# Kernel tuning notes

Hardware: AMD Instinct MI355X
Metric: run time of the kernel (lower is better)

Reference implementation:

```python
import jax, jax.numpy as jnp
import numpy as np

N_HEAD = 16
ROPE_BASE = 10000.0


def _rope_tables(T, head_dim, dtype=jnp.float32):
    inv_freq = 1.0 / (ROPE_BASE ** (jnp.arange(0, head_dim, 2, dtype=jnp.float32) / head_dim))
    t = jnp.arange(T, dtype=jnp.float32)
    freqs = t[:, None] * inv_freq[None, :]          # [T, D/2]
    emb = jnp.concatenate([freqs, freqs], axis=-1)  # [T, D]
    return jnp.cos(emb).astype(dtype), jnp.sin(emb).astype(dtype)


def _rotate_half(x):
    d = x.shape[-1] // 2
    return jnp.concatenate([-x[..., d:], x[..., :d]], axis=-1)


def setup_inputs() -> dict:
    key = jax.random.key(0)
    ks = jax.random.split(key, 5)
    B, T, C = 2, 2048, 2048
    s = 1.0 / np.sqrt(C)
    return {
        "x": jax.random.normal(ks[0], (B, T, C), dtype=jnp.float32),
        "wq": jax.random.normal(ks[1], (C, C), dtype=jnp.float32) * s,
        "wk": jax.random.normal(ks[2], (C, C), dtype=jnp.float32) * s,
        "wv": jax.random.normal(ks[3], (C, C), dtype=jnp.float32) * s,
        "wo": jax.random.normal(ks[4], (C, C), dtype=jnp.float32) * s,
    }


def reference(x, wq, wk, wv, wo):
    B, T, C = x.shape
    H = N_HEAD
    D = C // H

    def heads(y):  # [B,T,C] -> [B,H,T,D]
        return y.reshape(B, T, H, D).transpose(0, 2, 1, 3)

    q = heads(x @ wq)
    k = heads(x @ wk)
    v = heads(x @ wv)

    cos, sin = _rope_tables(T, D, x.dtype)          # [T, D]
    cos = cos[None, None, :, :]
    sin = sin[None, None, :, :]
    q = q * cos + _rotate_half(q) * sin
    k = k * cos + _rotate_half(k) * sin

    scale = 1.0 / np.sqrt(D)
    scores = jnp.einsum('bhqd,bhkd->bhqk', q, k) * scale   # [B,H,T,T]
    causal = jnp.tril(jnp.ones((T, T), dtype=bool))
    scores = jnp.where(causal[None, None, :, :], scores, jnp.finfo(scores.dtype).min)
    attn = jax.nn.softmax(scores, axis=-1)
    y = jnp.einsum('bhqk,bhkd->bhqd', attn, v)             # [B,H,T,D]
    y = y.transpose(0, 2, 1, 3).reshape(B, T, C)
    return y @ wo
```

## Files before the change

kernel.cpp:

```cpp
#include <hip/hip_runtime.h>
#include <hip/hip_bf16.h>
#include <math.h>


#define TT 2048
#define CCn 2048
#define HH 16
#define DD 128
#define MMr 4096
#define NQKV 6144

typedef __attribute__((ext_vector_type(8))) short s16x8;
typedef __attribute__((ext_vector_type(4))) short s16x4;
typedef __attribute__((ext_vector_type(4))) float f32x4;

__device__ __forceinline__ short bf16_of(float f) {
  unsigned u = __float_as_uint(f);
  unsigned r = u + 0x7fffu + ((u >> 16) & 1u);
  return (short)(r >> 16);
}
__device__ __forceinline__ float f_of_bf16(short s) {
  return __uint_as_float(((unsigned)(unsigned short)s) << 16);
}
__device__ __forceinline__ float ex2(float x) { return exp2f(x); }

__device__ __forceinline__ void lds_load16(const void* g, void* l) {
  __builtin_amdgcn_global_load_lds((__attribute__((address_space(1))) void*)g,
                                   (__attribute__((address_space(3))) void*)l,
                                   16, 0, 0);
}

__global__ __launch_bounds__(256) void k_tables(float* __restrict__ cosT,
                                                float* __restrict__ sinT) {
  int idx = blockIdx.x * 256 + threadIdx.x;
  int t = idx >> 6, i = idx & 63;
  float inv = powf(10000.0f, -(float)i * (1.0f / 64.0f));
  float f = (float)t * inv;
  cosT[idx] = cosf(f);
  sinT[idx] = sinf(f);
}

__global__ __launch_bounds__(256) void k_cast_x(const float* __restrict__ x,
                                                short* __restrict__ xb) {
  int i = blockIdx.x * 256 + threadIdx.x;
  f32x4 v = ((const f32x4*)x)[i];
  s16x4 o;
#pragma unroll
  for (int j = 0; j < 4; ++j) o[j] = bf16_of(v[j]);
  ((s16x4*)xb)[i] = o;
}

__global__ __launch_bounds__(256) void k_wtrans4(const float* __restrict__ w0,
                                                 const float* __restrict__ w1,
                                                 const float* __restrict__ w2,
                                                 const float* __restrict__ w3,
                                                 short* __restrict__ wqkvT,
                                                 short* __restrict__ woT) {
  __shared__ float tile[32][33];
  int z = blockIdx.z;
  const float* w = (z == 0) ? w0 : (z == 1) ? w1 : (z == 2) ? w2 : w3;
  short* wt = (z == 3) ? woT : wqkvT + (size_t)z * 2048 * 2048;
  int n0 = blockIdx.x * 32, k0 = blockIdx.y * 32;
  int tx = threadIdx.x & 31, ty = threadIdx.x >> 5;
#pragma unroll
  for (int j = 0; j < 4; ++j) {
    int k = ty * 4 + j;
    tile[k][tx] = w[(size_t)(k0 + k) * CCn + n0 + tx];
  }
  __syncthreads();
#pragma unroll
  for (int j = 0; j < 4; ++j) {
    int n = ty * 4 + j;
    wt[(size_t)(n0 + n) * CCn + k0 + tx] = bf16_of(tile[tx][n]);
  }
}

__global__ __launch_bounds__(256) void k_vtrans(const short* __restrict__ src,
                                                short* __restrict__ dst) {
  __shared__ short tile[32][33];
  int bh = blockIdx.y, b = bh >> 4, h = bh & 15;
  int dt = blockIdx.x & 3, tt = blockIdx.x >> 2;
  int tx = threadIdx.x & 31, ty = threadIdx.x >> 5;
  const short* sp = src + ((size_t)(b * TT + tt * 32)) * NQKV + 4096 + h * DD + dt * 32;
#pragma unroll
  for (int j = 0; j < 4; ++j) {
    int tr = ty * 4 + j;
    tile[tr][tx] = sp[(size_t)tr * NQKV + tx];
  }
  __syncthreads();
  short* dp = dst + ((size_t)(bh * DD + dt * 32)) * TT + tt * 32;
#pragma unroll
  for (int j = 0; j < 4; ++j) {
    int dr = ty * 4 + j;
    dp[(size_t)dr * TT + tx] = tile[tx][dr];
  }
}

__global__ __launch_bounds__(256) void k_rope2(const short* __restrict__ qkv,
                                               const float* __restrict__ cosT,
                                               const float* __restrict__ sinT,
                                               short* __restrict__ Qb,
                                               short* __restrict__ Kb, float kmul) {
  int which = blockIdx.y;
  int coff = which << 11;
  short* dstb = which ? Kb : Qb;
  float mul = which ? kmul : 1.0f;
  int idx = blockIdx.x * 256 + threadIdx.x;
  int i4 = (idx & 15) * 4;
  int h = (idx >> 4) & 15;
  int t = (idx >> 8) & 2047;
  int b = idx >> 19;
  const short* row = qkv + ((size_t)(b * TT + t)) * NQKV + coff + h * DD;
  s16x4 v0 = *(const s16x4*)(row + i4);
  s16x4 v1 = *(const s16x4*)(row + i4 + 64);
  f32x4 c4 = *(const f32x4*)(cosT + t * 64 + i4);
  f32x4 s4 = *(const f32x4*)(sinT + t * 64 + i4);
  s16x4 o0, o1;
#pragma unroll
  for (int j = 0; j < 4; ++j) {
    float a = f_of_bf16(v0[j]), bb = f_of_bf16(v1[j]);
    o0[j] = bf16_of((a * c4[j] - bb * s4[j]) * mul);
    o1[j] = bf16_of((bb * c4[j] + a * s4[j]) * mul);
  }
  short* orow = dstb + ((size_t)((b * HH + h) * TT + t)) * DD;
  *(s16x4*)(orow + i4) = o0;
  *(s16x4*)(orow + i4 + 64) = o1;
}

template <int WNF, bool BF16OUT>
__global__ __launch_bounds__(512) void k_g8(const short* __restrict__ A,
                                            const short* __restrict__ Bt,
                                            void* __restrict__ Cout,
                                            int M, int N, int K) {
  constexpr int BN = WNF * 64;
  constexpr int BHS = BN * 32;
  constexpr int NBL = WNF / 2;
  constexpr int VMN = 2 + WNF;
  __shared__ short smem[32768 + 4 * BHS];
  const int tid = threadIdx.x, wid = tid >> 6, lane = tid & 63;
  const int wm = wid >> 2, wn = wid & 3;
  const int lr = lane & 15, lk = lane >> 4;
  const int swz = (lk ^ ((lr >> 1) & 3)) * 8;

  int nwg = gridDim.x, orig = blockIdx.x;
  int xcd = orig & 7, bidx = orig >> 3;
  int q = nwg >> 3, rmd = nwg & 7;
  int wg = (xcd < rmd) ? (xcd * (q + 1) + bidx)
                       : (rmd * (q + 1) + (xcd - rmd) * q + bidx);
  const int NBM = M >> 8;
  const int m0 = (wg % NBM) * 256, n0 = (wg / NBM) * BN;

  auto stageA = [&](int buf, int ks, int kt) {
#pragma unroll
    for (int l = 0; l < 2; ++l) {
      int lin = l * 512 + tid;
      int row = lin >> 2;
      int cc = (lin & 3) ^ ((row >> 1) & 3);
      lds_load16(A + (size_t)(m0 + row) * K + kt * 64 + ks * 32 + cc * 8,
                 smem + buf * 16384 + ks * 8192 + lin * 8);
    }
  };
  auto stageB = [&](int buf, int ks, int kt) {
#pragma unroll
    for (int l = 0; l < NBL; ++l) {
      int lin = l * 512 + tid;
      int row = lin >> 2;
      int cc = (lin & 3) ^ ((row >> 1) & 3);
      lds_load16(Bt + (size_t)(n0 + row) * K + kt * 64 + ks * 32 + cc * 8,
                 smem + 32768 + buf * 2 * BHS + ks * BHS + lin * 8);
    }
  };

  s16x8 af[4], bfr[WNF];
  f32x4 acc[8][WNF] = {};

#define LDA(BUF, KS, MH)                                                       \
  _Pragma("unroll") for (int i = 0; i < 4; ++i) af[i] =                        \
      *(const s16x8*)(smem + (BUF) * 16384 + (KS) * 8192 +                     \
                      (wm * 128 + (MH) * 64 + i * 16 + lr) * 32 + swz);
#define LDB(BUF, KS)                                                           \
  _Pragma("unroll") for (int j = 0; j < WNF; ++j) bfr[j] =                     \
      *(const s16x8*)(smem + 32768 + (BUF) * 2 * BHS + (KS) * BHS +            \
                      (wn * (WNF * 16) + j * 16 + lr) * 32 + swz);
#define BAR_MFMA(MH)                                                           \
  __builtin_amdgcn_s_barrier();                                                \
  asm volatile("s_waitcnt lgkmcnt(0)" ::: "memory");                           \
  __builtin_amdgcn_s_setprio(1);                                               \
  _Pragma("unroll") for (int i = 0; i < 4; ++i)                                \
      _Pragma("unroll") for (int j = 0; j < WNF; ++j)                          \
      acc[(MH) * 4 + i][j] = __builtin_amdgcn_mfma_f32_16x16x32_bf16(          \
          af[i], bfr[j], acc[(MH) * 4 + i][j], 0, 0, 0);                       \
  __builtin_amdgcn_s_setprio(0);
#define VMW(cond)                                                              \
  if (cond) { asm volatile("s_waitcnt vmcnt(%0)" ::"i"(VMN) : "memory"); }     \
  else      { asm volatile("s_waitcnt vmcnt(0)" ::: "memory"); }

  const int nk = K >> 6, niter = nk >> 1;
  stageB(0, 0, 0); stageA(0, 0, 0); stageB(0, 1, 0); stageA(0, 1, 0);
  stageB(1, 0, 1); stageA(1, 0, 1); stageB(1, 1, 1);
  asm volatile("s_waitcnt vmcnt(%0)" ::"i"(VMN) : "memory");
  __builtin_amdgcn_s_barrier();

#pragma unroll 1
  for (int it = 0; it < niter; ++it) {
    const int kt1 = 2 * it + 1, kt2 = 2 * it + 2, kt3 = 2 * it + 3;
    const bool s2 = kt2 < nk, s3 = kt3 < nk;
    LDA(0, 0, 0); LDB(0, 0);
    stageA(1, 1, kt1);
    BAR_MFMA(0);
    __builtin_amdgcn_s_barrier();
    LDA(0, 0, 1);
    if (s2) stageB(0, 0, kt2);
    BAR_MFMA(1);
    __builtin_amdgcn_s_barrier();
    LDA(0, 1, 0); LDB(0, 1);
    if (s2) stageA(0, 0, kt2);
    BAR_MFMA(0);
    __builtin_amdgcn_s_barrier();
    LDA(0, 1, 1);
    if (s2) stageB(0, 1, kt2);
    BAR_MFMA(1);
    VMW(s2);
    __builtin_amdgcn_s_barrier();
    LDA(1, 0, 0); LDB(1, 0);
    if (s2) stageA(0, 1, kt2);
    BAR_MFMA(0);
    __builtin_amdgcn_s_barrier();
    LDA(1, 0, 1);
    if (s3) stageB(1, 0, kt3);
    BAR_MFMA(1);
    __builtin_amdgcn_s_barrier();
    LDA(1, 1, 0); LDB(1, 1);
    if (s3) stageA(1, 0, kt3);
    BAR_MFMA(0);
    __builtin_amdgcn_s_barrier();
    LDA(1, 1, 1);
    if (s3) stageB(1, 1, kt3);
    BAR_MFMA(1);
    VMW(s3);
    __builtin_amdgcn_s_barrier();
  }
#undef LDA
#undef LDB
#undef BAR_MFMA
#undef VMW

#pragma unroll
  for (int f = 0; f < 8; ++f)
#pragma unroll
    for (int j = 0; j < WNF; ++j) {
      int row0 = m0 + wm * 128 + (f >> 2) * 64 + (f & 3) * 16 + lk * 4;
      int col = n0 + wn * (WNF * 16) + j * 16 + lr;
#pragma unroll
      for (int rr = 0; rr < 4; ++rr) {
        if (BF16OUT)
          ((short*)Cout)[(size_t)(row0 + rr) * N + col] = bf16_of(acc[f][j][rr]);
        else
          ((float*)Cout)[(size_t)(row0 + rr) * N + col] = acc[f][j][rr];
      }
    }
}

__global__ __launch_bounds__(256) void k_attn(const short* __restrict__ Qb,
                                              const short* __restrict__ Kb,
                                              const short* __restrict__ Vt,
                                              short* __restrict__ yb) {
  __shared__ short Ks[2][64 * 128];
  __shared__ short Vs[128 * 64];
  __shared__ short Ps[4][16 * 72];
  const int tid = threadIdx.x, wid = tid >> 6, lane = tid & 63;
  const int lr = lane & 15, lk = lane >> 4;
  const int bh = blockIdx.y, bx = blockIdx.x;
  const size_t baseQK = (size_t)bh * TT * DD;
  const int b = bh >> 4, h = bh & 15;

  auto stageK = [&](int bi, int kt2) {
#pragma unroll
    for (int it = 0; it < 4; ++it) {
      int ch = it * 256 + tid;
      int r = ch >> 4, cc = ch & 15;
      int cs = cc ^ (r & 7);
      lds_load16(Kb + baseQK + (size_t)(kt2 * 64 + r) * DD + cs * 8,
                 &Ks[bi][(size_t)(it * 256 + wid * 64) * 8]);
    }
  };
  auto stageV = [&](int kt2) {
#pragma unroll
    for (int it = 0; it < 4; ++it) {
      int ch = it * 256 + tid;
      int d = ch >> 3, kc = ch & 7;
      int cs = kc ^ (d & 7);
      lds_load16(Vt + baseQK + (size_t)d * TT + kt2 * 64 + cs * 8,
                 &Vs[(size_t)(it * 256 + wid * 64) * 8]);
    }
  };

#pragma unroll 1
  for (int pass = 0; pass < 2; ++pass) {
    const int qt = pass ? (31 - bx) : bx;
    const int q0 = qt * 64;
    const int qg = q0 + wid * 16 + lr;
    s16x8 qf[4];
#pragma unroll
    for (int ds = 0; ds < 4; ++ds)
      qf[ds] = *(const s16x8*)(Qb + baseQK + (size_t)qg * DD + (ds * 4 + lk) * 8);

    float mrun = -3.0e38f, lrun = 0.f;
    f32x4 yacc[8] = {};

    const int nkt = qt + 1;
    stageK(0, 0);
    stageV(0);
    __syncthreads();
    int buf = 0;
#pragma unroll 1
    for (int kt = 0; kt < nkt; ++kt) {
      if (kt + 1 < nkt) stageK(buf ^ 1, kt + 1);
      f32x4 sf[4] = {};
#pragma unroll
      for (int sub = 0; sub < 4; ++sub) {
        int kr = sub * 16 + lr;
#pragma unroll
        for (int ds = 0; ds < 4; ++ds) {
          int cc = (ds * 4 + lk) ^ (kr & 7);
          s16x8 kf = *(const s16x8*)(&Ks[buf][kr * 128 + cc * 8]);
          sf[sub] = __builtin_amdgcn_mfma_f32_16x16x32_bf16(kf, qf[ds], sf[sub], 0, 0, 0);
        }
      }
      const int kvbase = kt * 64;
      if (kvbase + 63 > q0 + wid * 16) {
#pragma unroll
        for (int sub = 0; sub < 4; ++sub)
#pragma unroll
          for (int r = 0; r < 4; ++r) {
            int kv = kvbase + sub * 16 + lk * 4 + r;
            if (kv > qg) sf[sub][r] = -3.0e38f;
          }
      }
      float tmax = -3.0e38f;
#pragma unroll
      for (int sub = 0; sub < 4; ++sub)
#pragma unroll
        for (int r = 0; r < 4; ++r) tmax = fmaxf(tmax, sf[sub][r]);
      tmax = fmaxf(tmax, __shfl_xor(tmax, 16, 64));
      tmax = fmaxf(tmax, __shfl_xor(tmax, 32, 64));
      if (!__all(tmax <= mrun + 11.0f)) {
        float mnew = fmaxf(mrun, tmax);
        float alpha = ex2(mrun - mnew);
        mrun = mnew;
        lrun *= alpha;
        float ar[4];
#pragma unroll
        for (int r = 0; r < 4; ++r) ar[r] = __shfl(alpha, lk * 4 + r, 64);
#pragma unroll
        for (int dn = 0; dn < 8; ++dn)
#pragma unroll
          for (int r = 0; r < 4; ++r) yacc[dn][r] *= ar[r];
      }
      float psum = 0.f;
#pragma unroll
      for (int sub = 0; sub < 4; ++sub) {
        s16x4 pq;
#pragma unroll
        for (int r = 0; r < 4; ++r) {
          float p = ex2(sf[sub][r] - mrun);
          psum += p;
          pq[r] = bf16_of(p);
        }
        *(s16x4*)(&Ps[wid][lr * 72 + sub * 16 + lk * 4]) = pq;
      }
      psum += __shfl_xor(psum, 16, 64);
      psum += __shfl_xor(psum, 32, 64);
      lrun += psum;
      __syncthreads();
      s16x8 pf0 = *(const s16x8*)(&Ps[wid][lr * 72 + lk * 8]);
      s16x8 pf1 = *(const s16x8*)(&Ps[wid][lr * 72 + 32 + lk * 8]);
#pragma unroll
      for (int dn = 0; dn < 8; ++dn) {
        int d = dn * 16 + lr;
        s16x8 vf0 = *(const s16x8*)(&Vs[d * 64 + (lk ^ (d & 7)) * 8]);
        yacc[dn] = __builtin_amdgcn_mfma_f32_16x16x32_bf16(pf0, vf0, yacc[dn], 0, 0, 0);
        s16x8 vf1 = *(const s16x8*)(&Vs[d * 64 + ((4 + lk) ^ (d & 7)) * 8]);
        yacc[dn] = __builtin_amdgcn_mfma_f32_16x16x32_bf16(pf1, vf1, yacc[dn], 0, 0, 0);
      }
      __syncthreads();
      if (kt + 1 < nkt) stageV(kt + 1);
      buf ^= 1;
    }
    float linv = 1.f / lrun;
    float lr4[4];
#pragma unroll
    for (int r = 0; r < 4; ++r) lr4[r] = __shfl(linv, lk * 4 + r, 64);
#pragma unroll
    for (int dn = 0; dn < 8; ++dn)
#pragma unroll
      for (int r = 0; r < 4; ++r) {
        int t = q0 + wid * 16 + lk * 4 + r;
        int c = h * DD + dn * 16 + lr;
        yb[((size_t)(b * TT + t)) * CCn + c] = bf16_of(yacc[dn][r] * lr4[r]);
      }
  }
}

extern "C" void kernel_launch(void* const* d_in, const int* in_sizes, int n_in,
                              void* d_out, int out_size, void* d_ws, size_t ws_size,
                              hipStream_t stream) {
  const float* x = (const float*)d_in[0];
  const float* wq = (const float*)d_in[1];
  const float* wk = (const float*)d_in[2];
  const float* wv = (const float*)d_in[3];
  const float* wo = (const float*)d_in[4];
  float* out = (float*)d_out;
  char* ws = (char*)d_ws;

  short* xb = (short*)(ws + 0);
  short* wqkvT = (short*)(ws + 16777216);
  short* woT = (short*)(ws + 41943040);
  short* qkv = (short*)(ws + 50331648);
  short* yb = (short*)(ws + 50331648);
  short* Qb = (short*)(ws + 100663296);
  short* Kb = (short*)(ws + 117440512);
  short* Vt = (short*)(ws + 134217728);
  float* cosT = (float*)(ws + 150994944);
  float* sinT = (float*)(ws + 151519232);

  const float kmul = 1.4426950408889634f / sqrtf(128.0f);

  k_tables<<<512, 256, 0, stream>>>(cosT, sinT);
  k_cast_x<<<8192, 256, 0, stream>>>(x, xb);
  k_wtrans4<<<dim3(64, 64, 4), 256, 0, stream>>>(wq, wk, wv, wo, wqkvT, woT);

  k_g8<4, true><<<384, 512, 0, stream>>>(xb, wqkvT, qkv, MMr, NQKV, CCn);

  k_rope2<<<dim3(4096, 2), 256, 0, stream>>>(qkv, cosT, sinT, Qb, Kb, kmul);
  k_vtrans<<<dim3(256, 32), 256, 0, stream>>>(qkv, Vt);

  k_attn<<<dim3(16, 32), 256, 0, stream>>>(Qb, Kb, Vt, yb);

  k_g8<2, false><<<256, 512, 0, stream>>>(yb, woT, out, MMr, CCn, CCn);
}
```

Before: 405.1 us.

## Reshape GEMM tiles to 128xBN and widen attention blocks to 128 queries

```diff
diff --git a/kernel.cpp b/kernel.cpp
--- a/kernel.cpp
+++ b/kernel.cpp
@@ -133,10 +133,11 @@
                                             void* __restrict__ Cout,
                                             int M, int N, int K) {
   constexpr int BN = WNF * 64;
+  constexpr int AHS = 128 * 32;
   constexpr int BHS = BN * 32;
-  constexpr int NBL = WNF / 2;
-  constexpr int VMN = 2 + WNF;
-  __shared__ short smem[32768 + 4 * BHS];
+  constexpr int NBL = BN / 128;
+  constexpr int WNH = WNF / 2;
+  __shared__ short smem[4 * AHS + 4 * BHS];
   const int tid = threadIdx.x, wid = tid >> 6, lane = tid & 63;
   const int wm = wid >> 2, wn = wid & 3;
   const int lr = lane & 15, lk = lane >> 4;
@@ -147,18 +148,14 @@
   int q = nwg >> 3, rmd = nwg & 7;
   int wg = (xcd < rmd) ? (xcd * (q + 1) + bidx)
                        : (rmd * (q + 1) + (xcd - rmd) * q + bidx);
-  const int NBM = M >> 8;
-  const int m0 = (wg % NBM) * 256, n0 = (wg / NBM) * BN;
+  const int NBM = M >> 7;
+  const int m0 = (wg % NBM) * 128, n0 = (wg / NBM) * BN;
 
   auto stageA = [&](int buf, int ks, int kt) {
-#pragma unroll
-    for (int l = 0; l < 2; ++l) {
-      int lin = l * 512 + tid;
-      int row = lin >> 2;
-      int cc = (lin & 3) ^ ((row >> 1) & 3);
-      lds_load16(A + (size_t)(m0 + row) * K + kt * 64 + ks * 32 + cc * 8,
-                 smem + buf * 16384 + ks * 8192 + lin * 8);
-    }
+    int row = tid >> 2;
+    int cc = (tid & 3) ^ ((row >> 1) & 3);
+    lds_load16(A + (size_t)(m0 + row) * K + kt * 64 + ks * 32 + cc * 8,
+               smem + buf * 2 * AHS + ks * AHS + tid * 8);
   };
   auto stageB = [&](int buf, int ks, int kt) {
 #pragma unroll
@@ -167,77 +164,78 @@
       int row = lin >> 2;
       int cc = (lin & 3) ^ ((row >> 1) & 3);
       lds_load16(Bt + (size_t)(n0 + row) * K + kt * 64 + ks * 32 + cc * 8,
-                 smem + 32768 + buf * 2 * BHS + ks * BHS + lin * 8);
+                 smem + 4 * AHS + buf * 2 * BHS + ks * BHS + lin * 8);
     }
   };
 
-  s16x8 af[4], bfr[WNF];
-  f32x4 acc[8][WNF] = {};
-
-#define LDA(BUF, KS, MH)                                                       \
+  s16x8 af[4], bfr[WNH];
+  f32x4 acc[4][WNF] = {};
+
+#define LDA(BUF, KS)                                                           \
   _Pragma("unroll") for (int i = 0; i < 4; ++i) af[i] =                        \
-      *(const s16x8*)(smem + (BUF) * 16384 + (KS) * 8192 +                     \
-                      (wm * 128 + (MH) * 64 + i * 16 + lr) * 32 + swz);
-#define LDB(BUF, KS)                                                           \
-  _Pragma("unroll") for (int j = 0; j < WNF; ++j) bfr[j] =                     \
-      *(const s16x8*)(smem + 32768 + (BUF) * 2 * BHS + (KS) * BHS +            \
-                      (wn * (WNF * 16) + j * 16 + lr) * 32 + swz);
-#define BAR_MFMA(MH)                                                           \
+      *(const s16x8*)(smem + (BUF) * 2 * AHS + (KS) * AHS +                    \
+                      (wm * 64 + i * 16 + lr) * 32 + swz);
+#define LDB(BUF, KS, NH)                                                       \
+  _Pragma("unroll") for (int j = 0; j < WNH; ++j) bfr[j] =                     \
+      *(const s16x8*)(smem + 4 * AHS + (BUF) * 2 * BHS + (KS) * BHS +          \
+                      (wn * (WNF * 16) + ((NH) * WNH + j) * 16 + lr) * 32 +    \
+                      swz);
+#define BAR_MFMA(NH)                                                           \
   __builtin_amdgcn_s_barrier();                                                \
   asm volatile("s_waitcnt lgkmcnt(0)" ::: "memory");                           \
   __builtin_amdgcn_s_setprio(1);                                               \
   _Pragma("unroll") for (int i = 0; i < 4; ++i)                                \
-      _Pragma("unroll") for (int j = 0; j < WNF; ++j)                          \
-      acc[(MH) * 4 + i][j] = __builtin_amdgcn_mfma_f32_16x16x32_bf16(          \
-          af[i], bfr[j], acc[(MH) * 4 + i][j], 0, 0, 0);                       \
+      _Pragma("unroll") for (int j = 0; j < WNH; ++j)                          \
+      acc[i][(NH) * WNH + j] = __builtin_amdgcn_mfma_f32_16x16x32_bf16(        \
+          af[i], bfr[j], acc[i][(NH) * WNH + j], 0, 0, 0);                     \
   __builtin_amdgcn_s_setprio(0);
-#define VMW(cond)                                                              \
-  if (cond) { asm volatile("s_waitcnt vmcnt(%0)" ::"i"(VMN) : "memory"); }     \
+#define VMW(cond, NN)                                                          \
+  if (cond) { asm volatile("s_waitcnt vmcnt(%0)" ::"i"(NN) : "memory"); }      \
   else      { asm volatile("s_waitcnt vmcnt(0)" ::: "memory"); }
 
   const int nk = K >> 6, niter = nk >> 1;
-  stageB(0, 0, 0); stageA(0, 0, 0); stageB(0, 1, 0); stageA(0, 1, 0);
-  stageB(1, 0, 1); stageA(1, 0, 1); stageB(1, 1, 1);
-  asm volatile("s_waitcnt vmcnt(%0)" ::"i"(VMN) : "memory");
+  stageA(0, 0, 0); stageB(0, 0, 0);
+  stageA(0, 1, 0); stageB(0, 1, 0);
+  stageA(1, 0, 1); stageB(1, 0, 1);
+  asm volatile("s_waitcnt vmcnt(%0)" ::"i"(1 + NBL) : "memory");
   __builtin_amdgcn_s_barrier();
 
 #pragma unroll 1
   for (int it = 0; it < niter; ++it) {
     const int kt1 = 2 * it + 1, kt2 = 2 * it + 2, kt3 = 2 * it + 3;
     const bool s2 = kt2 < nk, s3 = kt3 < nk;
-    LDA(0, 0, 0); LDB(0, 0);
-    stageA(1, 1, kt1);
+    LDA(0, 0); LDB(0, 0, 0);
+    stageA(1, 1, kt1); stageB(1, 1, kt1);
     BAR_MFMA(0);
     __builtin_amdgcn_s_barrier();
-    LDA(0, 0, 1);
+    LDB(0, 0, 1);
+    if (s2) stageA(0, 0, kt2);
+    BAR_MFMA(1);
+    __builtin_amdgcn_s_barrier();
+    LDA(0, 1); LDB(0, 1, 0);
     if (s2) stageB(0, 0, kt2);
+    BAR_MFMA(0);
+    __builtin_amdgcn_s_barrier();
+    LDB(0, 1, 1);
+    if (s2) stageA(0, 1, kt2);
     BAR_MFMA(1);
-    __builtin_amdgcn_s_barrier();
-    LDA(0, 1, 0); LDB(0, 1);
-    if (s2) stageA(0, 0, kt2);
+    VMW(s2, 2 + NBL);
+    __builtin_amdgcn_s_barrier();
+    LDA(1, 0); LDB(1, 0, 0);
+    if (s2) stageB(0, 1, kt2);
     BAR_MFMA(0);
     __builtin_amdgcn_s_barrier();
-    LDA(0, 1, 1);
-    if (s2) stageB(0, 1, kt2);
+    LDB(1, 0, 1);
+    if (s3) stageA(1, 0, kt3);
     BAR_MFMA(1);
-    VMW(s2);
-    __builtin_amdgcn_s_barrier();
-    LDA(1, 0, 0); LDB(1, 0);
-    if (s2) stageA(0, 1, kt2);
+    __builtin_amdgcn_s_barrier();
+    LDA(1, 1); LDB(1, 1, 0);
+    if (s3) stageB(1, 0, kt3);
     BAR_MFMA(0);
     __builtin_amdgcn_s_barrier();
-    LDA(1, 0, 1);
-    if (s3) stageB(1, 0, kt3);
+    LDB(1, 1, 1);
     BAR_MFMA(1);
-    __builtin_amdgcn_s_barrier();
-    LDA(1, 1, 0); LDB(1, 1);
-    if (s3) stageA(1, 0, kt3);
-    BAR_MFMA(0);
-    __builtin_amdgcn_s_barrier();
-    LDA(1, 1, 1);
-    if (s3) stageB(1, 1, kt3);
-    BAR_MFMA(1);
-    VMW(s3);
+    VMW(s3, 1 + NBL);
     __builtin_amdgcn_s_barrier();
   }
 #undef LDA
@@ -246,28 +244,28 @@
 #undef VMW
 
 #pragma unroll
-  for (int f = 0; f < 8; ++f)
+  for (int i = 0; i < 4; ++i)
 #pragma unroll
     for (int j = 0; j < WNF; ++j) {
-      int row0 = m0 + wm * 128 + (f >> 2) * 64 + (f & 3) * 16 + lk * 4;
+      int row0 = m0 + wm * 64 + i * 16 + lk * 4;
       int col = n0 + wn * (WNF * 16) + j * 16 + lr;
 #pragma unroll
       for (int rr = 0; rr < 4; ++rr) {
         if (BF16OUT)
-          ((short*)Cout)[(size_t)(row0 + rr) * N + col] = bf16_of(acc[f][j][rr]);
+          ((short*)Cout)[(size_t)(row0 + rr) * N + col] = bf16_of(acc[i][j][rr]);
         else
-          ((float*)Cout)[(size_t)(row0 + rr) * N + col] = acc[f][j][rr];
+          ((float*)Cout)[(size_t)(row0 + rr) * N + col] = acc[i][j][rr];
       }
     }
 }
 
-__global__ __launch_bounds__(256) void k_attn(const short* __restrict__ Qb,
+__global__ __launch_bounds__(512) void k_attn(const short* __restrict__ Qb,
                                               const short* __restrict__ Kb,
                                               const short* __restrict__ Vt,
                                               short* __restrict__ yb) {
   __shared__ short Ks[2][64 * 128];
   __shared__ short Vs[128 * 64];
-  __shared__ short Ps[4][16 * 72];
+  __shared__ short Ps[8][16 * 72];
   const int tid = threadIdx.x, wid = tid >> 6, lane = tid & 63;
   const int lr = lane & 15, lk = lane >> 4;
   const int bh = blockIdx.y, bx = blockIdx.x;
@@ -276,29 +274,29 @@
 
   auto stageK = [&](int bi, int kt2) {
 #pragma unroll
-    for (int it = 0; it < 4; ++it) {
-      int ch = it * 256 + tid;
+    for (int it = 0; it < 2; ++it) {
+      int ch = it * 512 + tid;
       int r = ch >> 4, cc = ch & 15;
       int cs = cc ^ (r & 7);
       lds_load16(Kb + baseQK + (size_t)(kt2 * 64 + r) * DD + cs * 8,
-                 &Ks[bi][(size_t)(it * 256 + wid * 64) * 8]);
+                 &Ks[bi][(size_t)(it * 512 + wid * 64) * 8]);
     }
   };
   auto stageV = [&](int kt2) {
 #pragma unroll
-    for (int it = 0; it < 4; ++it) {
-      int ch = it * 256 + tid;
+    for (int it = 0; it < 2; ++it) {
+      int ch = it * 512 + tid;
       int d = ch >> 3, kc = ch & 7;
       int cs = kc ^ (d & 7);
       lds_load16(Vt + baseQK + (size_t)d * TT + kt2 * 64 + cs * 8,
-                 &Vs[(size_t)(it * 256 + wid * 64) * 8]);
+                 &Vs[(size_t)(it * 512 + wid * 64) * 8]);
     }
   };
 
 #pragma unroll 1
   for (int pass = 0; pass < 2; ++pass) {
-    const int qt = pass ? (31 - bx) : bx;
-    const int q0 = qt * 64;
+    const int qt = pass ? (15 - bx) : bx;
+    const int q0 = qt * 128;
     const int qg = q0 + wid * 16 + lr;
     s16x8 qf[4];
 #pragma unroll
@@ -308,7 +306,7 @@
     float mrun = -3.0e38f, lrun = 0.f;
     f32x4 yacc[8] = {};
 
-    const int nkt = qt + 1;
+    const int nkt = 2 * qt + 2;
     stageK(0, 0);
     stageV(0);
     __syncthreads();
@@ -430,12 +428,12 @@
   k_cast_x<<<8192, 256, 0, stream>>>(x, xb);
   k_wtrans4<<<dim3(64, 64, 4), 256, 0, stream>>>(wq, wk, wv, wo, wqkvT, woT);
 
-  k_g8<4, true><<<384, 512, 0, stream>>>(xb, wqkvT, qkv, MMr, NQKV, CCn);
+  k_g8<6, true><<<512, 512, 0, stream>>>(xb, wqkvT, qkv, MMr, NQKV, CCn);
 
   k_rope2<<<dim3(4096, 2), 256, 0, stream>>>(qkv, cosT, sinT, Qb, Kb, kmul);
   k_vtrans<<<dim3(256, 32), 256, 0, stream>>>(qkv, Vt);
 
-  k_attn<<<dim3(16, 32), 256, 0, stream>>>(Qb, Kb, Vt, yb);
-
-  k_g8<2, false><<<256, 512, 0, stream>>>(yb, woT, out, MMr, CCn, CCn);
-}
+  k_attn<<<dim3(8, 32), 512, 0, stream>>>(Qb, Kb, Vt, yb);
+
+  k_g8<4, false><<<256, 512, 0, stream>>>(yb, woT, out, MMr, CCn, CCn);
+}
```

Result: no change. 399.4 us (-1.4%).
